# Kernel tuning notes

Hardware: AMD Instinct MI355X
Metric: run time of the kernel (lower is better)

Reference implementation:

```python
import jax, jax.numpy as jnp
import numpy as np

SCALE = 64 ** 0.5  # hardcoded in original module regardless of dims


def setup_inputs() -> dict:
    key = jax.random.key(0)
    kx, kw = jax.random.split(key)
    B, S, D, O = 8, 2048, 512, 512
    x = jax.random.normal(kx, (B, S, D), dtype=jnp.float32)
    kernel = jax.random.normal(kw, (3, D, O), dtype=jnp.float32) * 0.02
    return {"x": x, "kernel": kernel}


def reference(x, kernel):
    # x: [B, S, D], kernel: [3, D, O]
    WQ = jnp.einsum('bsd,do->bso', x, kernel[0])
    WK = jnp.einsum('bsd,do->bso', x, kernel[1])
    WV = jnp.einsum('bsd,do->bso', x, kernel[2])
    QK = jnp.einsum('bso,bto->bst', WQ, WK)  # [B, S, S]
    # argmin of row-sums, taken from batch element 0 and applied to all batches
    # (faithful to c[0] in the original TF code)
    row_sums = jnp.sum(QK, axis=2)          # [B, S]
    c0 = jnp.argmin(row_sums[0])            # scalar index
    # Original removes row c0, scales, softmaxes remaining rows over last axis,
    # then re-inserts a zero row at c0. Softmax is row-independent, so this is
    # equivalent to softmax on all rows followed by zeroing row c0.
    A = jax.nn.softmax(QK / SCALE, axis=-1)  # [B, S, S]
    row_mask = (jnp.arange(QK.shape[1]) == c0)[None, :, None]
    A = jnp.where(row_mask, jnp.zeros((), A.dtype), A)
    V = jnp.einsum('bst,bto->bso', A, WV)    # [B, S, O]
    return V
```

## Files before the change

### kernel.cpp

```cpp
#include <hip/hip_runtime.h>
#include <stdint.h>

typedef __attribute__((ext_vector_type(8))) short short8;
typedef __attribute__((ext_vector_type(4))) float f32x4;

__device__ __forceinline__ float bf2f(unsigned short u) {
  union { unsigned int i; float f; } x; x.i = ((unsigned int)u) << 16; return x.f;
}
__device__ __forceinline__ unsigned short f2bf(float f) {
  union { float f; unsigned int i; } x; x.f = f;
  unsigned int u = x.i;
  unsigned int r = (u + 0x7FFFu + ((u >> 16) & 1u)) >> 16;
  return (unsigned short)r;
}
__device__ __forceinline__ unsigned int fmono(float f) {
  unsigned int u = __float_as_uint(f);
  return (u & 0x80000000u) ? ~u : (u | 0x80000000u);
}

typedef const __attribute__((address_space(1))) void* gas_ptr;
typedef __attribute__((address_space(3))) void* las_ptr;
__device__ __forceinline__ void gld_lds16(const void* g, void* l) {
  __builtin_amdgcn_global_load_lds((gas_ptr)g, (las_ptr)l, 16, 0, 0);
}

__global__ void cvt_x_kernel(const float* __restrict__ x, unsigned short* __restrict__ xbf, int n8) {
  int i = blockIdx.x * blockDim.x + threadIdx.x;
  if (i >= n8) return;
  const float4* xp = (const float4*)x;
  float4 a = xp[2 * i], b = xp[2 * i + 1];
  union { unsigned short us[8]; uint4 v; } o;
  o.us[0] = f2bf(a.x); o.us[1] = f2bf(a.y); o.us[2] = f2bf(a.z); o.us[3] = f2bf(a.w);
  o.us[4] = f2bf(b.x); o.us[5] = f2bf(b.y); o.us[6] = f2bf(b.z); o.us[7] = f2bf(b.w);
  ((uint4*)xbf)[i] = o.v;
}

__global__ void cvt_w_kernel(const float* __restrict__ kern, unsigned short* __restrict__ wbfT) {
  __shared__ float tile[32][33];
  int w = blockIdx.z;
  int d0 = blockIdx.x * 32, o0 = blockIdx.y * 32;
  int c = threadIdx.x & 31, r0 = threadIdx.x >> 5;
  const float* kp = kern + (size_t)w * 262144;
  unsigned short* op = wbfT + (size_t)w * 262144;
#pragma unroll
  for (int i = 0; i < 4; ++i)
    tile[r0 + 8 * i][c] = kp[(size_t)(d0 + r0 + 8 * i) * 512 + o0 + c];
  __syncthreads();
#pragma unroll
  for (int i = 0; i < 4; ++i)
    op[(size_t)(o0 + r0 + 8 * i) * 512 + d0 + c] = f2bf(tile[c][r0 + 8 * i]);
}

template <int MODE, int BNT>
__global__ __launch_bounds__(512, 1) void gemm8p(
    const unsigned short* __restrict__ A, const unsigned short* __restrict__ B,
    void* __restrict__ C, int M, int N, int K,
    long long Abat, long long Bbat, long long Cbat, float scale,
    const float* __restrict__ aux1) {
  constexpr int NF = BNT / 64;
  constexpr int LB = BNT / 128;
  constexpr int BHB = (BNT / 2) * 128;
  constexpr int PBUF = 32768 + 2 * BHB;
  __shared__ __align__(16) char lds[2 * PBUF];

  const int tx = N / BNT, ty = M >> 8;
  const int nwg = gridDim.x;
  const int bid = blockIdx.x;
  const int swz = (bid & 7) * (nwg >> 3) + (bid >> 3);
  const int tpz = tx * ty;
  const int z = swz / tpz;
  const int rem = swz - z * tpz;
  const int by = rem / tx;
  const int bx = rem - by * tx;
  const unsigned short* Ab = A + (size_t)z * (size_t)Abat;
  const unsigned short* Bb = B + (size_t)z * (size_t)Bbat;
  const int bm0 = by << 8;
  const int bn0 = bx * BNT;

  const int tid = threadIdx.x, lane = tid & 63, w = tid >> 6;
  const int wr = w >> 2, wc = w & 3;
  const int ln15 = lane & 15, hi = lane >> 4;
  const unsigned xorv = (unsigned)(lane & 7) << 4;
  const unsigned K2 = (unsigned)K * 2;

  const char* gsrc[4];
  gsrc[0] = (const char*)(Ab + (size_t)bm0 * K);
  gsrc[1] = (const char*)(Ab + (size_t)(bm0 + 128) * K);
  gsrc[2] = (const char*)(Bb + (size_t)bn0 * K);
  gsrc[3] = (const char*)(Bb + (size_t)(bn0 + BNT / 2) * K);
  const int hoff_[4] = {0, 16384, 32768, 32768 + BHB};
  unsigned op0 = (unsigned)(w * 1024 + lane * 16);
  unsigned op1 = op0 + 8192;
  const unsigned soff0 = (op0 >> 7) * K2 + ((op0 & 127) ^ (((op0 >> 7) & 7) << 4));
  const unsigned soff1 = (op1 >> 7) * K2 + ((op1 & 127) ^ (((op1 >> 7) & 7) << 4));
  const int lb0 = w * 1024, lb1 = 8192 + w * 1024;

#define STAGE(h, pp, kb)                                              \
  do {                                                                \
    char* lp_ = lds + (pp) * PBUF + hoff_[h];                         \
    const char* gp_ = gsrc[h] + ((unsigned)(kb) << 1);                \
    gld_lds16(gp_ + soff0, lp_ + lb0);                                \
    if ((h) < 2 || LB == 2) gld_lds16(gp_ + soff1, lp_ + lb1);        \
  } while (0)

  f32x4 acc[8][NF];
#pragma unroll
  for (int i = 0; i < 8; ++i)
#pragma unroll
    for (int j = 0; j < NF; ++j) acc[i][j] = (f32x4){0.f, 0.f, 0.f, 0.f};

  const int NT = K >> 6;
  STAGE(0, 0, 0);
  STAGE(1, 0, 0);
  STAGE(2, 0, 0);
  STAGE(3, 0, 0);
  asm volatile("s_waitcnt vmcnt(0)" ::: "memory");
  __builtin_amdgcn_s_barrier();

  short8 bfrag[NF][2];
  for (int t = 0; t < NT; ++t) {
    const int p = t & 1;
    char* Lp = lds + p * PBUF;
    const int kN = (t + 1) << 6;
    const bool sN = (t + 1 < NT);
#pragma unroll
    for (int q = 0; q < 4; ++q) {
      if (q == 0) {
#pragma unroll
        for (int nf = 0; nf < NF; ++nf)
#pragma unroll
          for (int k = 0; k < 2; ++k)
            bfrag[nf][k] = *(const short8*)(Lp + 32768 + (wc >> 1) * BHB +
                ((wc & 1) * (BNT / 4) + nf * 16 + ln15) * 128 +
                (((unsigned)(k * 64 + hi * 16)) ^ xorv));
      }
      short8 af[2][2];
#pragma unroll
      for (int i = 0; i < 2; ++i)
#pragma unroll
        for (int k = 0; k < 2; ++k)
          af[i][k] = *(const short8*)(Lp + wr * 16384 +
              ((q * 2 + i) * 16 + ln15) * 128 +
              (((unsigned)(k * 64 + hi * 16)) ^ xorv));
      if (q == 0 && sN) { STAGE(0, p ^ 1, kN); STAGE(2, p ^ 1, kN); }
      if (q == 1 && sN) { STAGE(1, p ^ 1, kN); STAGE(3, p ^ 1, kN); }
      __builtin_amdgcn_s_setprio(1);
#pragma unroll
      for (int i = 0; i < 2; ++i)
#pragma unroll
        for (int nf = 0; nf < NF; ++nf)
#pragma unroll
          for (int k = 0; k < 2; ++k)
            acc[q * 2 + i][nf] = __builtin_amdgcn_mfma_f32_16x16x32_bf16(
                af[i][k], bfrag[nf][k], acc[q * 2 + i][nf], 0, 0, 0);
      __builtin_amdgcn_s_setprio(0);
    }
    asm volatile("s_waitcnt vmcnt(0) lgkmcnt(0)" ::: "memory");
    __builtin_amdgcn_s_barrier();
  }
#undef STAGE

  const int rg = hi * 4;
  const int cc = ln15;
#pragma unroll
  for (int mf = 0; mf < 8; ++mf) {
#pragma unroll
    for (int nf = 0; nf < NF; ++nf) {
#pragma unroll
      for (int r = 0; r < 4; ++r) {
        int m = bm0 + wr * 128 + mf * 16 + rg + r;
        int n = bn0 + wc * (BNT / 4) + nf * 16 + cc;
        float v = acc[mf][nf][r];
        if (MODE == 0) {
          ((unsigned short*)C)[(size_t)z * (size_t)Cbat + (size_t)m * N + n] =
              f2bf(__expf(v * scale));
        } else if (MODE == 1) {
          int bb = n >> 11, tl = n & 2047;
          ((unsigned short*)C)[((size_t)(bb * 512 + m) << 11) + tl] = f2bf(v);
        } else if (MODE == 2) {
          float lv = aux1[(size_t)z * 2048 + m];
          ((float*)C)[(size_t)z * (size_t)Cbat + (size_t)m * N + n] = v * lv;
        } else {
          size_t idx = (size_t)(n >> 9) * 8388608 + (size_t)m * 512 + (n & 511);
          float sc = (n >> 9) ? 1.0f : 0.125f;
          ((unsigned short*)C)[idx] = f2bf(v * sc);
        }
      }
    }
  }
}

__global__ void ksum_kernel(const unsigned short* __restrict__ WK, float* __restrict__ partial) {
  int col = threadIdx.x;
  int t0 = blockIdx.x * 64;
  float s = 0.f;
  for (int t = 0; t < 64; ++t) s += bf2f(WK[(size_t)(t0 + t) * 512 + col]);
  partial[blockIdx.x * 512 + col] = s;
}

__global__ void rs_argmin_kernel(const unsigned short* __restrict__ WQ,
                                 const float* __restrict__ partial,
                                 unsigned long long* __restrict__ key) {
  __shared__ __align__(16) float ks[512];
  int tid = threadIdx.x;
  for (int c = tid; c < 512; c += 256) {
    float s = 0.f;
#pragma unroll
    for (int j = 0; j < 32; ++j) s += partial[j * 512 + c];
    ks[c] = s;
  }
  __syncthreads();
  int w = tid >> 6, lane = tid & 63;
  float4 ka = *(const float4*)&ks[lane * 8];
  float4 kb = *(const float4*)&ks[lane * 8 + 4];
  for (int it = 0; it < 16; ++it) {
    int row = blockIdx.x * 64 + w * 16 + it;
    uint4 q = *(const uint4*)(WQ + (size_t)row * 512 + lane * 8);
    float d = 0.f;
    d += bf2f((unsigned short)(q.x & 0xffff)) * ka.x;
    d += bf2f((unsigned short)(q.x >> 16)) * ka.y;
    d += bf2f((unsigned short)(q.y & 0xffff)) * ka.z;
    d += bf2f((unsigned short)(q.y >> 16)) * ka.w;
    d += bf2f((unsigned short)(q.z & 0xffff)) * kb.x;
    d += bf2f((unsigned short)(q.z >> 16)) * kb.y;
    d += bf2f((unsigned short)(q.w & 0xffff)) * kb.z;
    d += bf2f((unsigned short)(q.w >> 16)) * kb.w;
#pragma unroll
    for (int m = 32; m; m >>= 1) d += __shfl_xor(d, m);
    if (lane == 0) {
      unsigned long long kk = ((unsigned long long)fmono(d) << 32) | (unsigned int)row;
      atomicMin(key, kk);
    }
  }
}

__global__ void rowsum_kernel(const unsigned short* __restrict__ S,
                              const unsigned long long* __restrict__ keyp,
                              float* __restrict__ linv) {
  int w = threadIdx.x >> 6, lane = threadIdx.x & 63;
  int row = blockIdx.x * 4 + w;
  const unsigned short* rowp = S + ((size_t)blockIdx.y * 2048 + row) * 2048;
  float s = 0.f;
#pragma unroll
  for (int i = 0; i < 4; ++i) {
    uint4 v = *(const uint4*)(rowp + i * 512 + lane * 8);
    s += bf2f((unsigned short)(v.x & 0xffff)) + bf2f((unsigned short)(v.x >> 16));
    s += bf2f((unsigned short)(v.y & 0xffff)) + bf2f((unsigned short)(v.y >> 16));
    s += bf2f((unsigned short)(v.z & 0xffff)) + bf2f((unsigned short)(v.z >> 16));
    s += bf2f((unsigned short)(v.w & 0xffff)) + bf2f((unsigned short)(v.w >> 16));
  }
#pragma unroll
  for (int k = 32; k; k >>= 1) s += __shfl_xor(s, k);
  if (lane == 0) {
    int c0 = (int)(unsigned int)(*keyp & 0xffffffffULL);
    linv[(size_t)blockIdx.y * 2048 + row] = (row == c0) ? 0.f : (1.f / s);
  }
}

extern "C" void kernel_launch(void* const* d_in, const int* in_sizes, int n_in,
                              void* d_out, int out_size, void* d_ws, size_t ws_size,
                              hipStream_t stream) {
  const float* x = (const float*)d_in[0];
  const float* kern = (const float*)d_in[1];
  float* out = (float*)d_out;

  char* ws = (char*)d_ws;
  size_t off = 0;
  auto alloc = [&](size_t b) -> char* {
    char* p = ws + off;
    off += (b + 255) & ~(size_t)255;
    return p;
  };
  unsigned short* xbf = (unsigned short*)alloc(16384ull * 512 * 2);
  unsigned short* wbfT = (unsigned short*)alloc(3ull * 512 * 512 * 2);
  unsigned short* WQ = (unsigned short*)alloc(16384ull * 512 * 2);
  unsigned short* WK = (unsigned short*)alloc(16384ull * 512 * 2);
  unsigned short* VT = (unsigned short*)alloc(16384ull * 512 * 2);
  float* partial = (float*)alloc(32ull * 512 * 4);
  unsigned long long* key = (unsigned long long*)alloc(256);
  float* linv = (float*)alloc(8ull * 2048 * 4);
  size_t fixed = off;
  size_t sbytes = 2048ull * 2048 * 2;
  int nb = 1;
  if (ws_size > fixed + sbytes) {
    size_t av = (ws_size - fixed) / sbytes;
    nb = av > 8 ? 8 : (int)av;
    if (nb < 1) nb = 1;
  }
  unsigned short* S = (unsigned short*)alloc(sbytes * (size_t)nb);

  hipMemsetAsync(key, 0xFF, 8, stream);

  cvt_x_kernel<<<4096, 256, 0, stream>>>(x, xbf, 1048576);
  cvt_w_kernel<<<dim3(16, 16, 3), 256, 0, stream>>>(kern, wbfT);

  gemm8p<3, 256><<<256, 512, 0, stream>>>(xbf, wbfT, WQ, 16384, 1024, 512, 0, 0, 0, 1.0f,
                                          nullptr);
  gemm8p<1, 128><<<256, 512, 0, stream>>>(wbfT + 524288, xbf, VT, 512, 16384, 512, 0, 0, 0, 1.0f,
                                          nullptr);

  ksum_kernel<<<32, 512, 0, stream>>>(WK, partial);
  rs_argmin_kernel<<<32, 256, 0, stream>>>(WQ, partial, key);

  for (int b0 = 0; b0 < 8; b0 += nb) {
    int cb = (8 - b0) < nb ? (8 - b0) : nb;
    gemm8p<0, 256><<<64 * cb, 512, 0, stream>>>(
        WQ + (size_t)b0 * 2048 * 512, WK + (size_t)b0 * 2048 * 512, S,
        2048, 2048, 512, 2048ll * 512, 2048ll * 512, 2048ll * 2048, 1.0f,
        nullptr);
    rowsum_kernel<<<dim3(512, cb), 256, 0, stream>>>(S, key, linv + (size_t)b0 * 2048);
    gemm8p<2, 128><<<32 * cb, 512, 0, stream>>>(
        S, VT + (size_t)b0 * 512 * 2048, out + (size_t)b0 * 2048 * 512,
        2048, 512, 2048, 2048ll * 2048, 512ll * 2048, 2048ll * 512, 1.0f,
        linv + (size_t)b0 * 2048);
  }
}
```

Baseline: 176.5 us.

## Replace 256-row GEMM tiles with 128x128 tiles at two blocks per CU

The templated GEMM moves from 256xBNT output tiles computed by 8 waves to 128x128 tiles computed by 4 waves, with launch bounds allowing two workgroups per CU. LDS per block shrinks and all GEMM launches get proportionally more workgroups. The aim is better load balance and latency hiding through higher occupancy. In exchange, each tile reuses loaded data less, so global and LDS traffic per FLOP rises.

```diff
diff --git a/kernel.cpp b/kernel.cpp
--- a/kernel.cpp
+++ b/kernel.cpp
@@ -51,19 +51,16 @@
     op[(size_t)(o0 + r0 + 8 * i) * 512 + d0 + c] = f2bf(tile[c][r0 + 8 * i]);
 }
 
-template <int MODE, int BNT>
-__global__ __launch_bounds__(512, 1) void gemm8p(
+template <int MODE>
+__global__ __launch_bounds__(256, 2) void gemm128(
     const unsigned short* __restrict__ A, const unsigned short* __restrict__ B,
     void* __restrict__ C, int M, int N, int K,
     long long Abat, long long Bbat, long long Cbat, float scale,
     const float* __restrict__ aux1) {
-  constexpr int NF = BNT / 64;
-  constexpr int LB = BNT / 128;
-  constexpr int BHB = (BNT / 2) * 128;
-  constexpr int PBUF = 32768 + 2 * BHB;
+  constexpr int PBUF = 32768;
   __shared__ __align__(16) char lds[2 * PBUF];
 
-  const int tx = N / BNT, ty = M >> 8;
+  const int tx = N >> 7, ty = M >> 7;
   const int nwg = gridDim.x;
   const int bid = blockIdx.x;
   const int swz = (bid & 7) * (nwg >> 3) + (bid >> 3);
@@ -74,40 +71,39 @@
   const int bx = rem - by * tx;
   const unsigned short* Ab = A + (size_t)z * (size_t)Abat;
   const unsigned short* Bb = B + (size_t)z * (size_t)Bbat;
-  const int bm0 = by << 8;
-  const int bn0 = bx * BNT;
+  const int bm0 = by << 7;
+  const int bn0 = bx << 7;
 
   const int tid = threadIdx.x, lane = tid & 63, w = tid >> 6;
-  const int wr = w >> 2, wc = w & 3;
+  const int wr = w >> 1, wc = w & 1;
   const int ln15 = lane & 15, hi = lane >> 4;
   const unsigned xorv = (unsigned)(lane & 7) << 4;
   const unsigned K2 = (unsigned)K * 2;
 
   const char* gsrc[4];
   gsrc[0] = (const char*)(Ab + (size_t)bm0 * K);
-  gsrc[1] = (const char*)(Ab + (size_t)(bm0 + 128) * K);
+  gsrc[1] = (const char*)(Ab + (size_t)(bm0 + 64) * K);
   gsrc[2] = (const char*)(Bb + (size_t)bn0 * K);
-  gsrc[3] = (const char*)(Bb + (size_t)(bn0 + BNT / 2) * K);
-  const int hoff_[4] = {0, 16384, 32768, 32768 + BHB};
-  unsigned op0 = (unsigned)(w * 1024 + lane * 16);
-  unsigned op1 = op0 + 8192;
+  gsrc[3] = (const char*)(Bb + (size_t)(bn0 + 64) * K);
+  const int hoff_[4] = {0, 8192, 16384, 24576};
+  const unsigned op0 = (unsigned)(tid * 16);
+  const unsigned op1 = op0 + 4096;
   const unsigned soff0 = (op0 >> 7) * K2 + ((op0 & 127) ^ (((op0 >> 7) & 7) << 4));
   const unsigned soff1 = (op1 >> 7) * K2 + ((op1 & 127) ^ (((op1 >> 7) & 7) << 4));
-  const int lb0 = w * 1024, lb1 = 8192 + w * 1024;
 
 #define STAGE(h, pp, kb)                                              \
   do {                                                                \
     char* lp_ = lds + (pp) * PBUF + hoff_[h];                         \
     const char* gp_ = gsrc[h] + ((unsigned)(kb) << 1);                \
-    gld_lds16(gp_ + soff0, lp_ + lb0);                                \
-    if ((h) < 2 || LB == 2) gld_lds16(gp_ + soff1, lp_ + lb1);        \
+    gld_lds16(gp_ + soff0, lp_ + op0);                                \
+    gld_lds16(gp_ + soff1, lp_ + op1);                                \
   } while (0)
 
-  f32x4 acc[8][NF];
-#pragma unroll
-  for (int i = 0; i < 8; ++i)
-#pragma unroll
-    for (int j = 0; j < NF; ++j) acc[i][j] = (f32x4){0.f, 0.f, 0.f, 0.f};
+  f32x4 acc[4][4];
+#pragma unroll
+  for (int i = 0; i < 4; ++i)
+#pragma unroll
+    for (int j = 0; j < 4; ++j) acc[i][j] = (f32x4){0.f, 0.f, 0.f, 0.f};
 
   const int NT = K >> 6;
   STAGE(0, 0, 0);
@@ -117,7 +113,7 @@
   asm volatile("s_waitcnt vmcnt(0)" ::: "memory");
   __builtin_amdgcn_s_barrier();
 
-  short8 bfrag[NF][2];
+  short8 bfrag[4][2];
   for (int t = 0; t < NT; ++t) {
     const int p = t & 1;
     char* Lp = lds + p * PBUF;
@@ -127,32 +123,28 @@
     for (int q = 0; q < 4; ++q) {
       if (q == 0) {
 #pragma unroll
-        for (int nf = 0; nf < NF; ++nf)
+        for (int nf = 0; nf < 4; ++nf)
 #pragma unroll
           for (int k = 0; k < 2; ++k)
-            bfrag[nf][k] = *(const short8*)(Lp + 32768 + (wc >> 1) * BHB +
-                ((wc & 1) * (BNT / 4) + nf * 16 + ln15) * 128 +
+            bfrag[nf][k] = *(const short8*)(Lp + 16384 +
+                (wc * 64 + nf * 16 + ln15) * 128 +
                 (((unsigned)(k * 64 + hi * 16)) ^ xorv));
       }
-      short8 af[2][2];
-#pragma unroll
-      for (int i = 0; i < 2; ++i)
-#pragma unroll
-        for (int k = 0; k < 2; ++k)
-          af[i][k] = *(const short8*)(Lp + wr * 16384 +
-              ((q * 2 + i) * 16 + ln15) * 128 +
-              (((unsigned)(k * 64 + hi * 16)) ^ xorv));
+      short8 af[2];
+#pragma unroll
+      for (int k = 0; k < 2; ++k)
+        af[k] = *(const short8*)(Lp +
+            (wr * 64 + q * 16 + ln15) * 128 +
+            (((unsigned)(k * 64 + hi * 16)) ^ xorv));
       if (q == 0 && sN) { STAGE(0, p ^ 1, kN); STAGE(2, p ^ 1, kN); }
       if (q == 1 && sN) { STAGE(1, p ^ 1, kN); STAGE(3, p ^ 1, kN); }
       __builtin_amdgcn_s_setprio(1);
 #pragma unroll
-      for (int i = 0; i < 2; ++i)
-#pragma unroll
-        for (int nf = 0; nf < NF; ++nf)
-#pragma unroll
-          for (int k = 0; k < 2; ++k)
-            acc[q * 2 + i][nf] = __builtin_amdgcn_mfma_f32_16x16x32_bf16(
-                af[i][k], bfrag[nf][k], acc[q * 2 + i][nf], 0, 0, 0);
+      for (int nf = 0; nf < 4; ++nf)
+#pragma unroll
+        for (int k = 0; k < 2; ++k)
+          acc[q][nf] = __builtin_amdgcn_mfma_f32_16x16x32_bf16(
+              af[k], bfrag[nf][k], acc[q][nf], 0, 0, 0);
       __builtin_amdgcn_s_setprio(0);
     }
     asm volatile("s_waitcnt vmcnt(0) lgkmcnt(0)" ::: "memory");
@@ -163,13 +155,13 @@
   const int rg = hi * 4;
   const int cc = ln15;
 #pragma unroll
-  for (int mf = 0; mf < 8; ++mf) {
-#pragma unroll
-    for (int nf = 0; nf < NF; ++nf) {
+  for (int mf = 0; mf < 4; ++mf) {
+#pragma unroll
+    for (int nf = 0; nf < 4; ++nf) {
 #pragma unroll
       for (int r = 0; r < 4; ++r) {
-        int m = bm0 + wr * 128 + mf * 16 + rg + r;
-        int n = bn0 + wc * (BNT / 4) + nf * 16 + cc;
+        int m = bm0 + wr * 64 + mf * 16 + rg + r;
+        int n = bn0 + wc * 64 + nf * 16 + cc;
         float v = acc[mf][nf][r];
         if (MODE == 0) {
           ((unsigned short*)C)[(size_t)z * (size_t)Cbat + (size_t)m * N + n] =
@@ -294,22 +286,22 @@
   cvt_x_kernel<<<4096, 256, 0, stream>>>(x, xbf, 1048576);
   cvt_w_kernel<<<dim3(16, 16, 3), 256, 0, stream>>>(kern, wbfT);
 
-  gemm8p<3, 256><<<256, 512, 0, stream>>>(xbf, wbfT, WQ, 16384, 1024, 512, 0, 0, 0, 1.0f,
-                                          nullptr);
-  gemm8p<1, 128><<<256, 512, 0, stream>>>(wbfT + 524288, xbf, VT, 512, 16384, 512, 0, 0, 0, 1.0f,
-                                          nullptr);
+  gemm128<3><<<1024, 256, 0, stream>>>(xbf, wbfT, WQ, 16384, 1024, 512, 0, 0, 0, 1.0f,
+                                       nullptr);
+  gemm128<1><<<512, 256, 0, stream>>>(wbfT + 524288, xbf, VT, 512, 16384, 512, 0, 0, 0, 1.0f,
+                                      nullptr);
 
   ksum_kernel<<<32, 512, 0, stream>>>(WK, partial);
   rs_argmin_kernel<<<32, 256, 0, stream>>>(WQ, partial, key);
 
   for (int b0 = 0; b0 < 8; b0 += nb) {
     int cb = (8 - b0) < nb ? (8 - b0) : nb;
-    gemm8p<0, 256><<<64 * cb, 512, 0, stream>>>(
+    gemm128<0><<<256 * cb, 256, 0, stream>>>(
         WQ + (size_t)b0 * 2048 * 512, WK + (size_t)b0 * 2048 * 512, S,
         2048, 2048, 512, 2048ll * 512, 2048ll * 512, 2048ll * 2048, 1.0f,
         nullptr);
     rowsum_kernel<<<dim3(512, cb), 256, 0, stream>>>(S, key, linv + (size_t)b0 * 2048);
-    gemm8p<2, 128><<<32 * cb, 512, 0, stream>>>(
+    gemm128<2><<<64 * cb, 256, 0, stream>>>(
         S, VT + (size_t)b0 * 512 * 2048, out + (size_t)b0 * 2048 * 512,
         2048, 512, 2048, 2048ll * 2048, 512ll * 2048, 2048ll * 512, 1.0f,
         linv + (size_t)b0 * 2048);
```

New measurement: 178.6 us. No clear change (+1.2%).

## Fuse softmax rowsum into PV GEMM via ones-vector MFMA

Applied to the files above, without the earlier changes.

Removes the separate rowsum kernel that re-read the full exp-score matrix. The PV GEMM computes each row's normalizer with extra MFMAs of the A fragments against a bf16 ones vector, and applies the argmin-row mask in its epilogue. This saves a full pass over S and one launch per batch chunk, at the cost of about 50% more MFMA issue in the PV GEMM and redundant rowsum computation across N-tiles.

```diff
diff --git a/kernel.cpp b/kernel.cpp
--- a/kernel.cpp
+++ b/kernel.cpp
@@ -56,7 +56,7 @@
     const unsigned short* __restrict__ A, const unsigned short* __restrict__ B,
     void* __restrict__ C, int M, int N, int K,
     long long Abat, long long Bbat, long long Cbat, float scale,
-    const float* __restrict__ aux1) {
+    const unsigned long long* __restrict__ keyp) {
   constexpr int NF = BNT / 64;
   constexpr int LB = BNT / 128;
   constexpr int BHB = (BNT / 2) * 128;
@@ -109,6 +109,15 @@
 #pragma unroll
     for (int j = 0; j < NF; ++j) acc[i][j] = (f32x4){0.f, 0.f, 0.f, 0.f};
 
+  f32x4 accs1[8];
+  short8 onesf;
+  if constexpr (MODE == 2) {
+#pragma unroll
+    for (int i = 0; i < 8; ++i) accs1[i] = (f32x4){0.f, 0.f, 0.f, 0.f};
+#pragma unroll
+    for (int j = 0; j < 8; ++j) onesf[j] = (short)0x3F80;
+  }
+
   const int NT = K >> 6;
   STAGE(0, 0, 0);
   STAGE(1, 0, 0);
@@ -146,13 +155,20 @@
       if (q == 1 && sN) { STAGE(1, p ^ 1, kN); STAGE(3, p ^ 1, kN); }
       __builtin_amdgcn_s_setprio(1);
 #pragma unroll
-      for (int i = 0; i < 2; ++i)
+      for (int i = 0; i < 2; ++i) {
 #pragma unroll
         for (int nf = 0; nf < NF; ++nf)
 #pragma unroll
           for (int k = 0; k < 2; ++k)
             acc[q * 2 + i][nf] = __builtin_amdgcn_mfma_f32_16x16x32_bf16(
                 af[i][k], bfrag[nf][k], acc[q * 2 + i][nf], 0, 0, 0);
+        if constexpr (MODE == 2) {
+#pragma unroll
+          for (int k = 0; k < 2; ++k)
+            accs1[q * 2 + i] = __builtin_amdgcn_mfma_f32_16x16x32_bf16(
+                af[i][k], onesf, accs1[q * 2 + i], 0, 0, 0);
+        }
+      }
       __builtin_amdgcn_s_setprio(0);
     }
     asm volatile("s_waitcnt vmcnt(0) lgkmcnt(0)" ::: "memory");
@@ -162,6 +178,8 @@
 
   const int rg = hi * 4;
   const int cc = ln15;
+  int c0 = 0;
+  if constexpr (MODE == 2) c0 = (int)(unsigned int)(*keyp & 0xffffffffULL);
 #pragma unroll
   for (int mf = 0; mf < 8; ++mf) {
 #pragma unroll
@@ -178,7 +196,7 @@
           int bb = n >> 11, tl = n & 2047;
           ((unsigned short*)C)[((size_t)(bb * 512 + m) << 11) + tl] = f2bf(v);
         } else if (MODE == 2) {
-          float lv = aux1[(size_t)z * 2048 + m];
+          float lv = (m == c0) ? 0.f : (1.f / accs1[mf][r]);
           ((float*)C)[(size_t)z * (size_t)Cbat + (size_t)m * N + n] = v * lv;
         } else {
           size_t idx = (size_t)(n >> 9) * 8388608 + (size_t)m * 512 + (n & 511);
@@ -234,29 +252,6 @@
   }
 }
 
-__global__ void rowsum_kernel(const unsigned short* __restrict__ S,
-                              const unsigned long long* __restrict__ keyp,
-                              float* __restrict__ linv) {
-  int w = threadIdx.x >> 6, lane = threadIdx.x & 63;
-  int row = blockIdx.x * 4 + w;
-  const unsigned short* rowp = S + ((size_t)blockIdx.y * 2048 + row) * 2048;
-  float s = 0.f;
-#pragma unroll
-  for (int i = 0; i < 4; ++i) {
-    uint4 v = *(const uint4*)(rowp + i * 512 + lane * 8);
-    s += bf2f((unsigned short)(v.x & 0xffff)) + bf2f((unsigned short)(v.x >> 16));
-    s += bf2f((unsigned short)(v.y & 0xffff)) + bf2f((unsigned short)(v.y >> 16));
-    s += bf2f((unsigned short)(v.z & 0xffff)) + bf2f((unsigned short)(v.z >> 16));
-    s += bf2f((unsigned short)(v.w & 0xffff)) + bf2f((unsigned short)(v.w >> 16));
-  }
-#pragma unroll
-  for (int k = 32; k; k >>= 1) s += __shfl_xor(s, k);
-  if (lane == 0) {
-    int c0 = (int)(unsigned int)(*keyp & 0xffffffffULL);
-    linv[(size_t)blockIdx.y * 2048 + row] = (row == c0) ? 0.f : (1.f / s);
-  }
-}
-
 extern "C" void kernel_launch(void* const* d_in, const int* in_sizes, int n_in,
                               void* d_out, int out_size, void* d_ws, size_t ws_size,
                               hipStream_t stream) {
@@ -278,7 +273,6 @@
   unsigned short* VT = (unsigned short*)alloc(16384ull * 512 * 2);
   float* partial = (float*)alloc(32ull * 512 * 4);
   unsigned long long* key = (unsigned long long*)alloc(256);
-  float* linv = (float*)alloc(8ull * 2048 * 4);
   size_t fixed = off;
   size_t sbytes = 2048ull * 2048 * 2;
   int nb = 1;
@@ -308,10 +302,9 @@
         WQ + (size_t)b0 * 2048 * 512, WK + (size_t)b0 * 2048 * 512, S,
         2048, 2048, 512, 2048ll * 512, 2048ll * 512, 2048ll * 2048, 1.0f,
         nullptr);
-    rowsum_kernel<<<dim3(512, cb), 256, 0, stream>>>(S, key, linv + (size_t)b0 * 2048);
     gemm8p<2, 128><<<32 * cb, 512, 0, stream>>>(
         S, VT + (size_t)b0 * 512 * 2048, out + (size_t)b0 * 2048 * 512,
         2048, 512, 2048, 2048ll * 2048, 512ll * 2048, 2048ll * 512, 1.0f,
-        linv + (size_t)b0 * 2048);
-  }
-}
+        key);
+  }
+}
```

Result: no change. 173.2 us (-1.9%).
